# Optimization experiments

Hardware: AMD Instinct MI355X
Metric: run time of the kernel (lower is better)

## Reference

```python
import jax, jax.numpy as jnp
import numpy as np

N = 262144
D = 512
B = 1024  # number of segments/graphs (batch.max()+1 in the torch code)


def setup_inputs() -> dict:
    key = jax.random.key(0)
    k1, k2, k3, k4 = jax.random.split(key, 4)
    x = jax.random.normal(k1, (N, D), dtype=jnp.float32)
    batch = jnp.sort(jax.random.randint(k2, (N,), 0, B, dtype=jnp.int64))
    # score MLP params: Linear(D, D//4) -> Tanh -> Linear(D//4, 1)
    W1 = jax.random.normal(k3, (D, D // 4), dtype=jnp.float32) * (1.0 / np.sqrt(D))
    b1 = jnp.zeros((D // 4,), dtype=jnp.float32)
    W2 = jax.random.normal(k4, (D // 4, 1), dtype=jnp.float32) * (1.0 / np.sqrt(D // 4))
    b2 = jnp.zeros((1,), dtype=jnp.float32)
    return {"x": x, "batch": batch, "W1": W1, "b1": b1, "W2": W2, "b2": b2}


def reference(x, batch, W1, b1, W2, b2):
    # score MLP (dropout inactive at inference)
    scores = jnp.tanh(x @ W1 + b1) @ W2 + b2              # [N, 1]
    scores = scores - jnp.max(scores)                      # global max-shift for stability
    exp_s = jnp.exp(scores)                                # [N, 1]
    denom = jax.ops.segment_sum(exp_s, batch, num_segments=B)  # [B, 1]
    weight = exp_s / (denom[batch] + 1e-8)                 # [N, 1] segment softmax
    out = jax.ops.segment_sum(weight * x, batch, num_segments=B)  # [B, D]
    return out
```

## Files before the change

### kernel.cpp

```cpp
#include <hip/hip_runtime.h>
#include <hip/hip_cooperative_groups.h>

namespace cg = cooperative_groups;

typedef _Float16 half8 __attribute__((ext_vector_type(8)));
typedef _Float16 half4v __attribute__((ext_vector_type(4)));
typedef float f32x4 __attribute__((ext_vector_type(4)));

#define LDK 72

__global__ void prep_w1t(const float* __restrict__ W1, _Float16* __restrict__ W1T) {
    int idx = blockIdx.x * 256 + threadIdx.x;
    int n = idx >> 9;
    int k = idx & 511;
    W1T[idx] = (_Float16)W1[k * 128 + n];
}

__global__ __launch_bounds__(256, 4) void fused_kernel(
        const float* __restrict__ x, const int* __restrict__ batch,
        const _Float16* __restrict__ W1T, const float* __restrict__ b1,
        const float* __restrict__ W2, const float* __restrict__ b2,
        float* __restrict__ scores, float* __restrict__ partial,
        float* __restrict__ denom, int* __restrict__ starts,
        float* __restrict__ out, int N, int NSEG, int ntiles)
{
    __shared__ __align__(16) _Float16 As[64][LDK];
    __shared__ __align__(16) _Float16 Bs[128][LDK];
    __shared__ float red[256];

    cg::grid_group gg = cg::this_grid();
    const int tid = threadIdx.x;
    const int wave = tid >> 6, lane = tid & 63;
    const int quad = lane >> 4, col = lane & 15;
    const long gsz = (long)gridDim.x * 256;
    const long gtid = (long)blockIdx.x * 256 + tid;

    float b1v[8], w2v[8];
    #pragma unroll
    for (int nt = 0; nt < 8; ++nt) {
        b1v[nt] = b1[nt * 16 + col];
        w2v[nt] = W2[nt * 16 + col];
    }
    const float bias2 = b2[0];
    float lmax = -1e30f;

    for (int tile = blockIdx.x; tile < ntiles; tile += gridDim.x) {
        const long row0 = (long)tile * 64;
        f32x4 acc[8] = {};
        for (int kc = 0; kc < 512; kc += 64) {
            #pragma unroll
            for (int it = 0; it < 4; ++it) {
                int idx = it * 256 + tid;
                int r = idx >> 4, c4 = idx & 15;
                float4 v = *(const float4*)&x[(row0 + r) * 512 + kc + c4 * 4];
                half4v h;
                h[0] = (_Float16)v.x; h[1] = (_Float16)v.y;
                h[2] = (_Float16)v.z; h[3] = (_Float16)v.w;
                *(half4v*)&As[r][c4 * 4] = h;
            }
            #pragma unroll
            for (int it = 0; it < 4; ++it) {
                int idx = it * 256 + tid;
                int n = idx >> 3, c8 = idx & 7;
                *(half8*)&Bs[n][c8 * 8] = *(const half8*)&W1T[n * 512 + kc + c8 * 8];
            }
            __syncthreads();
            #pragma unroll
            for (int ks = 0; ks < 64; ks += 32) {
                half8 a = *(half8*)&As[wave * 16 + col][ks + quad * 8];
                half8 bf[8];
                #pragma unroll
                for (int nt = 0; nt < 8; ++nt)
                    bf[nt] = *(half8*)&Bs[nt * 16 + col][ks + quad * 8];
                #pragma unroll
                for (int nt = 0; nt < 8; ++nt)
                    acc[nt] = __builtin_amdgcn_mfma_f32_16x16x32_f16(a, bf[nt], acc[nt], 0, 0, 0);
            }
            __syncthreads();
        }
        #pragma unroll
        for (int r = 0; r < 4; ++r) {
            float p = 0.f;
            #pragma unroll
            for (int nt = 0; nt < 8; ++nt)
                p += tanhf(acc[nt][r] + b1v[nt]) * w2v[nt];
            #pragma unroll
            for (int off = 1; off < 16; off <<= 1) p += __shfl_xor(p, off);
            p += bias2;
            lmax = fmaxf(lmax, p);
            if (col == 0) scores[row0 + wave * 16 + quad * 4 + r] = p;
        }
    }
    for (long i = gtid; i < N; i += gsz) {
        int s = batch[i];
        int pv = (i == 0) ? -1 : batch[i - 1];
        for (int bb = pv + 1; bb <= s; ++bb) starts[bb] = (int)i;
        if (i == N - 1)
            for (int bb = s + 1; bb <= NSEG; ++bb) starts[bb] = N;
    }
    for (long bb = gtid; bb < NSEG; bb += gsz) denom[bb] = 0.f;
    red[tid] = lmax;
    __syncthreads();
    for (int s = 128; s > 0; s >>= 1) {
        if (tid < s) red[tid] = fmaxf(red[tid], red[tid + s]);
        __syncthreads();
    }
    if (tid == 0) partial[blockIdx.x] = red[0];
    gg.sync();

    float m = -1e30f;
    for (int i = tid; i < (int)gridDim.x; i += 256) m = fmaxf(m, partial[i]);
    red[tid] = m;
    __syncthreads();
    for (int s = 128; s > 0; s >>= 1) {
        if (tid < s) red[tid] = fmaxf(red[tid], red[tid + s]);
        __syncthreads();
    }
    const float gm = red[0];
    for (long i = gtid; i < N; i += gsz) {
        int seg = batch[i];
        float e = __expf(scores[i] - gm);
        scores[i] = e;
        float v = e;
        #pragma unroll
        for (int off = 1; off < 64; off <<= 1) {
            float ov = __shfl_down(v, off);
            int os = __shfl_down(seg, off);
            if (lane + off < 64 && os == seg) v += ov;
        }
        int pseg = __shfl_up(seg, 1);
        if (lane == 0 || pseg != seg) atomicAdd(&denom[seg], v);
    }
    gg.sync();

    const int hh = tid >> 7;
    const int c4 = (tid & 127) * 4;
    float* comb = (float*)As;
    for (int b = blockIdx.x; b < NSEG; b += gridDim.x) {
        const int s0 = starts[b], s1 = starts[b + 1];
        const float dinv = 1.f / (denom[b] + 1e-8f);
        f32x4 acc = {};
        for (int i = s0 + hh; i < s1; i += 2) {
            float w = scores[i];
            const f32x4 xv = *(const f32x4*)&x[(long)i * 512 + c4];
            acc += w * xv;
        }
        __syncthreads();
        if (hh) *(f32x4*)&comb[c4] = acc;
        __syncthreads();
        if (!hh) {
            acc += *(f32x4*)&comb[c4];
            acc *= dinv;
            *(f32x4*)&out[(long)b * 512 + c4] = acc;
        }
    }
}

extern "C" void kernel_launch(void* const* d_in, const int* in_sizes, int n_in,
                              void* d_out, int out_size, void* d_ws, size_t ws_size,
                              hipStream_t stream) {
    const float* x     = (const float*)d_in[0];
    const int*   batch = (const int*)d_in[1];
    const float* W1    = (const float*)d_in[2];
    const float* b1    = (const float*)d_in[3];
    const float* W2    = (const float*)d_in[4];
    const float* b2    = (const float*)d_in[5];
    float* out = (float*)d_out;

    const int N = in_sizes[1];
    const int NSEG = out_size / 512;
    const int ntiles = N / 64;

    _Float16* W1T  = (_Float16*)d_ws;
    float* scores  = (float*)((char*)d_ws + 131072);
    float* partial = scores + N;
    float* denom   = partial + 1024;
    int*   starts  = (int*)(denom + NSEG);

    prep_w1t<<<256, 256, 0, stream>>>(W1, W1T);

    int nb = 0;
    if (hipOccupancyMaxActiveBlocksPerMultiprocessor(&nb, fused_kernel, 256, 0) != hipSuccess
        || nb < 1)
        nb = 4;
    long grid = (long)nb * 256;
    if (grid > 1024) grid = 1024;

    void* args[] = { (void*)&x, (void*)&batch, (void*)&W1T, (void*)&b1, (void*)&W2, (void*)&b2,
                     (void*)&scores, (void*)&partial, (void*)&denom, (void*)&starts,
                     (void*)&out, (void*)&N, (void*)&NSEG, (void*)&ntiles };
    hipLaunchCooperativeKernel((const void*)fused_kernel, dim3((int)grid), dim3(256),
                               args, 0, stream);
}
```

Baseline: 1.003 ms.

## Replace cooperative multi-phase kernel with single-pass fused score/softmax/aggregate using atomics

Drops the global max-shift and grid syncs. Each 64-row block loads its x tile once into LDS as fp16, computes scores via MFMA, exponentiates them, and atomically accumulates both the denominator and the weighted x sums into a zeroed workspace. A separate finalize kernel then divides by the denominator. This avoids re-reading x from HBM for the aggregation and removes the cooperative barriers, at the cost of many global float atomics, weighted sums computed from fp16 x, and possible overflow without the max shift.

```diff
diff --git a/kernel.cpp b/kernel.cpp
--- a/kernel.cpp
+++ b/kernel.cpp
@@ -1,127 +1,97 @@
 #include <hip/hip_runtime.h>
-#include <hip/hip_cooperative_groups.h>
-
-namespace cg = cooperative_groups;
 
 typedef _Float16 half8 __attribute__((ext_vector_type(8)));
 typedef _Float16 half4v __attribute__((ext_vector_type(4)));
 typedef float f32x4 __attribute__((ext_vector_type(4)));
 
-#define LDK 72
+#define NPAD 520
 
-__global__ void prep_w1t(const float* __restrict__ W1, _Float16* __restrict__ W1T) {
-    int idx = blockIdx.x * 256 + threadIdx.x;
-    int n = idx >> 9;
-    int k = idx & 511;
-    W1T[idx] = (_Float16)W1[k * 128 + n];
+__device__ __forceinline__ float tanh_fast(float v) {
+    float e = __expf(2.f * v);
+    return 1.f - 2.f / (e + 1.f);
 }
 
-__global__ __launch_bounds__(256, 4) void fused_kernel(
+__global__ void init_kernel(const float* __restrict__ W1, _Float16* __restrict__ W1T,
+                            float* __restrict__ zero_base, int nzero4) {
+    int b = blockIdx.x;
+    if (b < 256) {
+        int idx = b * 256 + threadIdx.x;
+        int n = idx >> 9, k = idx & 511;
+        W1T[idx] = (_Float16)W1[k * 128 + n];
+    } else {
+        f32x4 z = {};
+        for (int i = (b - 256) * 256 + threadIdx.x; i < nzero4; i += 256 * 256)
+            *(f32x4*)&zero_base[(long)i * 4] = z;
+    }
+}
+
+__global__ __launch_bounds__(256, 2) void fused_kernel(
         const float* __restrict__ x, const int* __restrict__ batch,
         const _Float16* __restrict__ W1T, const float* __restrict__ b1,
         const float* __restrict__ W2, const float* __restrict__ b2,
-        float* __restrict__ scores, float* __restrict__ partial,
-        float* __restrict__ denom, int* __restrict__ starts,
-        float* __restrict__ out, int N, int NSEG, int ntiles)
+        float* __restrict__ out_acc, float* __restrict__ denom)
 {
-    __shared__ __align__(16) _Float16 As[64][LDK];
-    __shared__ __align__(16) _Float16 Bs[128][LDK];
-    __shared__ float red[256];
+    __shared__ __align__(16) _Float16 As[64][NPAD];
+    __shared__ float exp_lds[64];
+    __shared__ int batch_lds[64];
 
-    cg::grid_group gg = cg::this_grid();
     const int tid = threadIdx.x;
-    const int wave = tid >> 6, lane = tid & 63;
+    const int wv = tid >> 6, lane = tid & 63;
     const int quad = lane >> 4, col = lane & 15;
-    const long gsz = (long)gridDim.x * 256;
-    const long gtid = (long)blockIdx.x * 256 + tid;
+    const long row0 = (long)blockIdx.x * 64;
 
-    float b1v[8], w2v[8];
-    #pragma unroll
-    for (int nt = 0; nt < 8; ++nt) {
-        b1v[nt] = b1[nt * 16 + col];
-        w2v[nt] = W2[nt * 16 + col];
+    if (tid < 64) batch_lds[tid] = (int)batch[row0 + tid];
+
+    #pragma unroll 8
+    for (int it = 0; it < 32; ++it) {
+        int f = it * 256 + tid;
+        int r = f >> 7, cf = f & 127;
+        float4 v = *(const float4*)&x[(row0 + r) * 512 + cf * 4];
+        half4v h;
+        h[0] = (_Float16)v.x; h[1] = (_Float16)v.y;
+        h[2] = (_Float16)v.z; h[3] = (_Float16)v.w;
+        *(half4v*)&As[r][cf * 4] = h;
     }
-    const float bias2 = b2[0];
-    float lmax = -1e30f;
+    __syncthreads();
 
-    for (int tile = blockIdx.x; tile < ntiles; tile += gridDim.x) {
-        const long row0 = (long)tile * 64;
-        f32x4 acc[8] = {};
-        for (int kc = 0; kc < 512; kc += 64) {
-            #pragma unroll
-            for (int it = 0; it < 4; ++it) {
-                int idx = it * 256 + tid;
-                int r = idx >> 4, c4 = idx & 15;
-                float4 v = *(const float4*)&x[(row0 + r) * 512 + kc + c4 * 4];
-                half4v h;
-                h[0] = (_Float16)v.x; h[1] = (_Float16)v.y;
-                h[2] = (_Float16)v.z; h[3] = (_Float16)v.w;
-                *(half4v*)&As[r][c4 * 4] = h;
-            }
-            #pragma unroll
-            for (int it = 0; it < 4; ++it) {
-                int idx = it * 256 + tid;
-                int n = idx >> 3, c8 = idx & 7;
-                *(half8*)&Bs[n][c8 * 8] = *(const half8*)&W1T[n * 512 + kc + c8 * 8];
-            }
-            __syncthreads();
-            #pragma unroll
-            for (int ks = 0; ks < 64; ks += 32) {
-                half8 a = *(half8*)&As[wave * 16 + col][ks + quad * 8];
-                half8 bf[8];
-                #pragma unroll
-                for (int nt = 0; nt < 8; ++nt)
-                    bf[nt] = *(half8*)&Bs[nt * 16 + col][ks + quad * 8];
-                #pragma unroll
-                for (int nt = 0; nt < 8; ++nt)
-                    acc[nt] = __builtin_amdgcn_mfma_f32_16x16x32_f16(a, bf[nt], acc[nt], 0, 0, 0);
-            }
-            __syncthreads();
+    f32x4 acc[8] = {};
+    #pragma unroll 4
+    for (int ks = 0; ks < 16; ++ks) {
+        half8 a = *(const half8*)&As[wv * 16 + col][ks * 32 + quad * 8];
+        half8 bf[8];
+        #pragma unroll
+        for (int nt = 0; nt < 8; ++nt)
+            bf[nt] = *(const half8*)&W1T[(nt * 16 + col) * 512 + ks * 32 + quad * 8];
+        #pragma unroll
+        for (int nt = 0; nt < 8; ++nt)
+            acc[nt] = __builtin_amdgcn_mfma_f32_16x16x32_f16(a, bf[nt], acc[nt], 0, 0, 0);
+    }
+
+    {
+        float b1v[8], w2v[8];
+        #pragma unroll
+        for (int nt = 0; nt < 8; ++nt) {
+            b1v[nt] = b1[nt * 16 + col];
+            w2v[nt] = W2[nt * 16 + col];
         }
+        const float bias2 = b2[0];
         #pragma unroll
         for (int r = 0; r < 4; ++r) {
             float p = 0.f;
             #pragma unroll
             for (int nt = 0; nt < 8; ++nt)
-                p += tanhf(acc[nt][r] + b1v[nt]) * w2v[nt];
+                p += tanh_fast(acc[nt][r] + b1v[nt]) * w2v[nt];
             #pragma unroll
             for (int off = 1; off < 16; off <<= 1) p += __shfl_xor(p, off);
-            p += bias2;
-            lmax = fmaxf(lmax, p);
-            if (col == 0) scores[row0 + wave * 16 + quad * 4 + r] = p;
+            if (col == 0)
+                exp_lds[wv * 16 + quad * 4 + r] = __expf(p + bias2);
         }
     }
-    for (long i = gtid; i < N; i += gsz) {
-        int s = batch[i];
-        int pv = (i == 0) ? -1 : batch[i - 1];
-        for (int bb = pv + 1; bb <= s; ++bb) starts[bb] = (int)i;
-        if (i == N - 1)
-            for (int bb = s + 1; bb <= NSEG; ++bb) starts[bb] = N;
-    }
-    for (long bb = gtid; bb < NSEG; bb += gsz) denom[bb] = 0.f;
-    red[tid] = lmax;
     __syncthreads();
-    for (int s = 128; s > 0; s >>= 1) {
-        if (tid < s) red[tid] = fmaxf(red[tid], red[tid + s]);
-        __syncthreads();
-    }
-    if (tid == 0) partial[blockIdx.x] = red[0];
-    gg.sync();
 
-    float m = -1e30f;
-    for (int i = tid; i < (int)gridDim.x; i += 256) m = fmaxf(m, partial[i]);
-    red[tid] = m;
-    __syncthreads();
-    for (int s = 128; s > 0; s >>= 1) {
-        if (tid < s) red[tid] = fmaxf(red[tid], red[tid + s]);
-        __syncthreads();
-    }
-    const float gm = red[0];
-    for (long i = gtid; i < N; i += gsz) {
-        int seg = batch[i];
-        float e = __expf(scores[i] - gm);
-        scores[i] = e;
-        float v = e;
+    if (tid < 64) {
+        int seg = batch_lds[tid];
+        float v = exp_lds[tid];
         #pragma unroll
         for (int off = 1; off < 64; off <<= 1) {
             float ov = __shfl_down(v, off);
@@ -129,31 +99,43 @@
             if (lane + off < 64 && os == seg) v += ov;
         }
         int pseg = __shfl_up(seg, 1);
-        if (lane == 0 || pseg != seg) atomicAdd(&denom[seg], v);
+        if (tid == 0 || pseg != seg) atomicAdd(&denom[seg], v);
     }
-    gg.sync();
 
-    const int hh = tid >> 7;
-    const int c4 = (tid & 127) * 4;
-    float* comb = (float*)As;
-    for (int b = blockIdx.x; b < NSEG; b += gridDim.x) {
-        const int s0 = starts[b], s1 = starts[b + 1];
-        const float dinv = 1.f / (denom[b] + 1e-8f);
-        f32x4 acc = {};
-        for (int i = s0 + hh; i < s1; i += 2) {
-            float w = scores[i];
-            const f32x4 xv = *(const f32x4*)&x[(long)i * 512 + c4];
-            acc += w * xv;
+    {
+        const int h2 = tid >> 7;
+        const int cg = tid & 127;
+        f32x4 wacc = {};
+        int cur = batch_lds[h2];
+        for (int j = h2; j < 64; j += 2) {
+            int s = batch_lds[j];
+            if (s != cur) {
+                #pragma unroll
+                for (int k2 = 0; k2 < 4; ++k2)
+                    atomicAdd(&out_acc[(long)cur * 512 + cg * 4 + k2], wacc[k2]);
+                wacc = (f32x4){};
+                cur = s;
+            }
+            float w = exp_lds[j];
+            half4v xh = *(const half4v*)&As[j][cg * 4];
+            wacc[0] += w * (float)xh[0];
+            wacc[1] += w * (float)xh[1];
+            wacc[2] += w * (float)xh[2];
+            wacc[3] += w * (float)xh[3];
         }
-        __syncthreads();
-        if (hh) *(f32x4*)&comb[c4] = acc;
-        __syncthreads();
-        if (!hh) {
-            acc += *(f32x4*)&comb[c4];
-            acc *= dinv;
-            *(f32x4*)&out[(long)b * 512 + c4] = acc;
-        }
+        #pragma unroll
+        for (int k2 = 0; k2 < 4; ++k2)
+            atomicAdd(&out_acc[(long)cur * 512 + cg * 4 + k2], wacc[k2]);
     }
+}
+
+__global__ void finalize_kernel(const float* __restrict__ out_acc,
+                                const float* __restrict__ denom,
+                                float* __restrict__ out) {
+    int i = blockIdx.x * 256 + threadIdx.x;
+    f32x4 v = *(const f32x4*)&out_acc[(long)i * 4];
+    float d = 1.f / (denom[i >> 7] + 1e-8f);
+    *(f32x4*)&out[(long)i * 4] = v * d;
 }
 
 extern "C" void kernel_launch(void* const* d_in, const int* in_sizes, int n_in,
@@ -169,26 +151,14 @@
 
     const int N = in_sizes[1];
     const int NSEG = out_size / 512;
-    const int ntiles = N / 64;
 
-    _Float16* W1T  = (_Float16*)d_ws;
-    float* scores  = (float*)((char*)d_ws + 131072);
-    float* partial = scores + N;
-    float* denom   = partial + 1024;
-    int*   starts  = (int*)(denom + NSEG);
+    _Float16* W1T   = (_Float16*)d_ws;
+    float* out_acc  = (float*)((char*)d_ws + 131072);
+    float* denom    = out_acc + (long)NSEG * 512;
 
-    prep_w1t<<<256, 256, 0, stream>>>(W1, W1T);
+    const int nzero4 = (NSEG * 512 + NSEG) / 4;
 
-    int nb = 0;
-    if (hipOccupancyMaxActiveBlocksPerMultiprocessor(&nb, fused_kernel, 256, 0) != hipSuccess
-        || nb < 1)
-        nb = 4;
-    long grid = (long)nb * 256;
-    if (grid > 1024) grid = 1024;
-
-    void* args[] = { (void*)&x, (void*)&batch, (void*)&W1T, (void*)&b1, (void*)&W2, (void*)&b2,
-                     (void*)&scores, (void*)&partial, (void*)&denom, (void*)&starts,
-                     (void*)&out, (void*)&N, (void*)&NSEG, (void*)&ntiles };
-    hipLaunchCooperativeKernel((const void*)fused_kernel, dim3((int)grid), dim3(256),
-                               args, 0, stream);
+    init_kernel<<<512, 256, 0, stream>>>(W1, W1T, out_acc, nzero4);
+    fused_kernel<<<N / 64, 256, 0, stream>>>(x, batch, W1T, b1, W2, b2, out_acc, denom);
+    finalize_kernel<<<out_size / 1024, 256, 0, stream>>>(out_acc, denom, out);
 }
```

After: 900.8 us. 1.11x faster.
